# Kernel optimization log

Hardware: AMD Instinct MI355X
Metric: run time of the kernel (lower is better)

The kernel has to match this reference:

```python
import jax, jax.numpy as jnp
import numpy as np

EPS = 1e-12  # F.normalize default eps

def _unfold3(x):
    # torch F.unfold(kernel=(3,3), padding=1): [B,C,H,W] -> [B, C*9, H*W]
    # channel-major, kernel offsets row-major (matches torch ordering)
    B, C, H, W = x.shape
    xp = jnp.pad(x, ((0, 0), (0, 0), (1, 1), (1, 1)))
    p = jnp.stack([xp[:, :, i:i + H, j:j + W] for i in range(3) for j in range(3)], axis=2)  # [B,C,9,H,W]
    return p.reshape(B, C * 9, H * W)

def _fold3(u, H, W):
    # torch F.fold(output_size=(H,W), kernel=(3,3), padding=1): sums overlapping patches
    B, CK, L = u.shape
    C = CK // 9
    p = u.reshape(B, C, 3, 3, H, W)
    out = jnp.zeros((B, C, H + 2, W + 2), u.dtype)
    for i in range(3):
        for j in range(3):
            out = out.at[:, :, i:i + H, j:j + W].add(p[:, :, i, j])
    return out[:, :, 1:H + 1, 1:W + 1]

def setup_inputs() -> dict:
    key = jax.random.key(0)
    k1, k2, k3 = jax.random.split(key, 3)
    B, C, H, W = 4, 64, 64, 64
    return {
        "lrsr_lv3": jax.random.normal(k1, (B, C, H, W), jnp.float32),
        "refsr_lv3": jax.random.normal(k2, (B, C, H, W), jnp.float32),
        "ref_lv3": jax.random.normal(k3, (B, C, H, W), jnp.float32),
    }

def reference(lrsr_lv3, refsr_lv3, ref_lv3):
    B, C, H, W = lrsr_lv3.shape
    lr_u = _unfold3(lrsr_lv3)                         # [B, D, L_lr], D = C*9
    rs_u = _unfold3(refsr_lv3).transpose(0, 2, 1)     # [B, L_ref, D]
    rs_u = rs_u / jnp.maximum(jnp.linalg.norm(rs_u, axis=2, keepdims=True), EPS)
    lr_u = lr_u / jnp.maximum(jnp.linalg.norm(lr_u, axis=1, keepdims=True), EPS)
    corr = jnp.einsum('brd,bdl->brl', rs_u, lr_u)     # [B, L_ref, L_lr]
    s = jnp.max(corr, axis=1)                         # [B, L_lr]
    arg = jnp.argmax(corr, axis=1)                    # [B, L_lr]
    ref_u = _unfold3(ref_lv3)                         # [B, D, L_ref]
    trans_u = jnp.take_along_axis(ref_u, arg[:, None, :], axis=2)  # [B, D, L_lr]
    trans_lv3 = _fold3(trans_u, H, W)                 # [B, C, H, W]
    return s.reshape(B, 1, H, W), trans_lv3
```

## Files before the change

kernel.cpp:

```cpp
#include <hip/hip_runtime.h>

#define BATCH 4
#define CH    64
#define HH    64
#define WW    64
#define LL    4096
#define SPLITS 8
#define RPS   512
#define BM    128
#define BN    128
#define NRT   (RPS/BM)

#define RSTB  96
#define BUFB  24576
#define BSOFF 12288
#define CSTRIDE 139392

#define PAD_L   4356
#define GP_BYTE_BASE 1376256
#define GP_SIDE_STRIDE 6690816
#define GP_B_STRIDE    1672704
#define GP_COMP_STRIDE 557568
#define GP_TOTAL       13381632

#define WS_SSQ_RS 0
#define WS_SSQ_LR 16384
#define WS_INV_RS 32768
#define WS_INV_LR 49152
#define WS_PMAX   65536
#define WS_PARG   196608
#define WS_ARG    327680

typedef __attribute__((ext_vector_type(8))) short short8b;
typedef __attribute__((ext_vector_type(4))) float f32x4;
typedef __attribute__((ext_vector_type(16))) float f32x16;

__device__ __forceinline__ void gload16(const void* g, void* l) {
    __builtin_amdgcn_global_load_lds(
        (const __attribute__((address_space(1))) unsigned int*)g,
        (__attribute__((address_space(3))) unsigned int*)l, 16, 0, 0);
}

__global__ void k_split(const float* __restrict__ lrsr,
                        const float* __restrict__ refsr,
                        float* __restrict__ ws) {
    int tid  = threadIdx.x;
    int pos  = blockIdx.x * 256 + tid;
    int c8   = blockIdx.y;
    int side = blockIdx.z >> 2;
    int b    = blockIdx.z & 3;
    const float* src = (side ? lrsr : refsr) + (size_t)b * CH * LL + c8 * 8 * LL + pos;
    int ppos = (pos >> 6) * 66 + (pos & 63) + 67;
    char* dst = (char*)ws + GP_BYTE_BASE + side * GP_SIDE_STRIDE + b * GP_B_STRIDE
              + (size_t)(c8 * PAD_L + ppos) * 16;
    union { unsigned short u[8]; uint4 v; } w0, w1, w2;
    #pragma unroll
    for (int cc = 0; cc < 8; ++cc) {
        float x = src[cc * LL];
        unsigned u0 = __float_as_uint(x);
        float f0 = __uint_as_float(u0 & 0xffff0000u);
        float r1 = x - f0;
        unsigned u1 = __float_as_uint(r1);
        float f1 = __uint_as_float(u1 & 0xffff0000u);
        float r2 = r1 - f1;
        w0.u[cc] = (unsigned short)(u0 >> 16);
        w1.u[cc] = (unsigned short)(u1 >> 16);
        w2.u[cc] = (unsigned short)(__float_as_uint(r2) >> 16);
    }
    *(uint4*)(dst)                      = w0.v;
    *(uint4*)(dst + GP_COMP_STRIDE)     = w1.v;
    *(uint4*)(dst + 2 * GP_COMP_STRIDE) = w2.v;
}

__global__ void k_ssq(const float* __restrict__ lrsr,
                      const float* __restrict__ refsr,
                      float* __restrict__ ws) {
    int t = blockIdx.x * 256 + threadIdx.x;
    int b = t >> 12;
    int r = t & (LL - 1);
    const float* pl = lrsr + (size_t)b * CH * LL + r;
    const float* pr = refsr + (size_t)b * CH * LL + r;
    float sl = 0.f, sr = 0.f;
    #pragma unroll 8
    for (int c = 0; c < CH; ++c) {
        float a = pl[c * LL]; sl += a * a;
        float d = pr[c * LL]; sr += d * d;
    }
    ws[WS_SSQ_RS + t] = sr;
    ws[WS_SSQ_LR + t] = sl;
}

__global__ void k_inv(float* __restrict__ ws) {
    int t = blockIdx.x * 256 + threadIdx.x;
    int b = t >> 12;
    int r = t & (LL - 1);
    int y = r >> 6, x = r & 63;
    float srs = 0.f, slr = 0.f;
    for (int di = -1; di <= 1; ++di) {
        int yy = y + di;
        if ((unsigned)yy >= (unsigned)HH) continue;
        for (int dj = -1; dj <= 1; ++dj) {
            int xx = x + dj;
            if ((unsigned)xx >= (unsigned)WW) continue;
            int idx = b * LL + yy * WW + xx;
            srs += ws[WS_SSQ_RS + idx];
            slr += ws[WS_SSQ_LR + idx];
        }
    }
    ws[WS_INV_RS + t] = 1.f / fmaxf(sqrtf(srs), 1e-12f);
    ws[WS_INV_LR + t] = 1.f / fmaxf(sqrtf(slr), 1e-12f);
}

__global__ __launch_bounds__(256, 3)
void k_corrmax(float* __restrict__ ws) {
    __shared__ __align__(16) char LDSB[2 * BUFB];

    int tid  = threadIdx.x;
    int b    = blockIdx.z;
    int bx   = blockIdx.x;
    int l0   = bx * BN;
    int rbs  = blockIdx.y * RPS;

    int lane = tid & 63;
    int w    = tid >> 6;
    int wr   = w >> 1;
    int wc   = w & 1;
    int l31  = lane & 31;
    int g2   = lane >> 5;

    const float* invn_rs = ws + WS_INV_RS + b * LL;
    const char*  gpB = (const char*)ws + GP_BYTE_BASE + b * GP_B_STRIDE;
    int sB = w & 1;
    const char* bp = gpB + sB * GP_SIDE_STRIDE;

    int LCb[6];
    #pragma unroll
    for (int n = 0; n < 6; ++n) {
        int gg   = (n * 2 + (w >> 1)) * 64 + lane;
        int row  = gg / 6;
        int slot = gg - row * 6;
        int comp = slot >> 1;
        int oct  = slot & 1;
        LCb[n] = comp * GP_COMP_STRIDE + oct * (PAD_L * 16)
               + (row + 2 * (row >> 6)) * 16;
    }
    int ldsw = sB * BSOFF + (w >> 1) * 1024;

    int abase = (wr * 64 + l31) * RSTB + g2 * 16;
    int bbase = BSOFF + (wc * 64 + l31) * RSTB + g2 * 16;

    int yb = rbs >> 6;
    int yB = bx * 2;

    auto issue = [&](int rt2, int q2, int m2, int bufo) {
        int i2 = (q2 < 3) ? -1 : ((q2 < 6) ? 0 : 1);
        int j2 = q2 - (i2 + 1) * 3 - 1;
        int suA = ((yb + rt2 * 2 + 1 + i2) * 66 + 1 + j2) * 16 + m2 * CSTRIDE;
        int suB = ((yB + 1 + i2) * 66 + 1 + j2) * 16 + m2 * CSTRIDE;
        int su  = sB ? suB : suA;
        #pragma unroll
        for (int n = 0; n < 6; ++n)
            gload16(bp + (LCb[n] + su), LDSB + bufo + ldsw + n * 2048);
    };

    float rm[2] = {-1e30f, -1e30f};
    int   ra[2] = {0, 0};

    issue(0, 0, 0, 0);
    __syncthreads();

    int cur = 0;
    for (int rt = 0; rt < NRT; ++rt) {
        int r0 = rbs + rt * BM;

        f32x16 acc[2][2];
        #pragma unroll
        for (int mf = 0; mf < 2; ++mf)
            #pragma unroll
            for (int nf = 0; nf < 2; ++nf)
                #pragma unroll
                for (int e = 0; e < 16; ++e) acc[mf][nf][e] = 0.f;

        for (int q = 0; q < 9; ++q) {
            #pragma unroll
            for (int m = 0; m < 4; ++m) {
                if (!(rt == NRT - 1 && q == 8 && m == 3)) {
                    int m2 = m + 1, q2 = q, rt2 = rt;
                    if (m2 == 4) { m2 = 0; ++q2; if (q2 == 9) { q2 = 0; ++rt2; } }
                    issue(rt2, q2, m2, (cur ^ 1) * BUFB);
                }
                const char* lb = LDSB + cur * BUFB;
                short8b a[2][3], bv[2][3];
                #pragma unroll
                for (int mf = 0; mf < 2; ++mf)
                    #pragma unroll
                    for (int c = 0; c < 3; ++c)
                        a[mf][c] = *(const short8b*)(lb + abase + mf * 3072 + c * 32);
                #pragma unroll
                for (int nf = 0; nf < 2; ++nf)
                    #pragma unroll
                    for (int c = 0; c < 3; ++c)
                        bv[nf][c] = *(const short8b*)(lb + bbase + nf * 3072 + c * 32);
                __builtin_amdgcn_s_setprio(1);
                #pragma unroll
                for (int mf = 0; mf < 2; ++mf)
                    #pragma unroll
                    for (int nf = 0; nf < 2; ++nf) {
                        f32x16 d = acc[mf][nf];
                        d = __builtin_amdgcn_mfma_f32_32x32x16_bf16(a[mf][0], bv[nf][0], d, 0, 0, 0);
                        d = __builtin_amdgcn_mfma_f32_32x32x16_bf16(a[mf][0], bv[nf][1], d, 0, 0, 0);
                        d = __builtin_amdgcn_mfma_f32_32x32x16_bf16(a[mf][1], bv[nf][0], d, 0, 0, 0);
                        d = __builtin_amdgcn_mfma_f32_32x32x16_bf16(a[mf][1], bv[nf][1], d, 0, 0, 0);
                        d = __builtin_amdgcn_mfma_f32_32x32x16_bf16(a[mf][0], bv[nf][2], d, 0, 0, 0);
                        d = __builtin_amdgcn_mfma_f32_32x32x16_bf16(a[mf][2], bv[nf][0], d, 0, 0, 0);
                        acc[mf][nf] = d;
                    }
                __builtin_amdgcn_s_setprio(0);
                __syncthreads();
                cur ^= 1;
            }
        }

        f32x4 inv4[2][4];
        #pragma unroll
        for (int mf = 0; mf < 2; ++mf)
            #pragma unroll
            for (int rb = 0; rb < 4; ++rb)
                inv4[mf][rb] = *(const f32x4*)&invn_rs[r0 + wr * 64 + mf * 32 + g2 * 4 + rb * 8];
        #pragma unroll
        for (int nf = 0; nf < 2; ++nf)
            #pragma unroll
            for (int mf = 0; mf < 2; ++mf)
                #pragma unroll
                for (int reg = 0; reg < 16; ++reg) {
                    int r = r0 + wr * 64 + mf * 32 + (reg & 3) + 8 * (reg >> 2) + 4 * g2;
                    float val = acc[mf][nf][reg] * inv4[mf][reg >> 2][reg & 3];
                    if (val > rm[nf] || (val == rm[nf] && r < ra[nf])) { rm[nf] = val; ra[nf] = r; }
                }
    }

    #pragma unroll
    for (int nf = 0; nf < 2; ++nf) {
        float ov = __shfl_xor(rm[nf], 32);
        int   oi = __shfl_xor(ra[nf], 32);
        if (ov > rm[nf] || (ov == rm[nf] && oi < ra[nf])) { rm[nf] = ov; ra[nf] = oi; }
    }
    __syncthreads();
    float* sm2 = (float*)LDSB;
    int*   si2 = (int*)LDSB + 256;
    if (lane < 32) {
        #pragma unroll
        for (int nf = 0; nf < 2; ++nf) {
            sm2[wr * 128 + wc * 64 + nf * 32 + l31] = rm[nf];
            si2[wr * 128 + wc * 64 + nf * 32 + l31] = ra[nf];
        }
    }
    __syncthreads();
    if (tid < 128) {
        float bm = sm2[tid]; int ba = si2[tid];
        float v  = sm2[128 + tid]; int a2 = si2[128 + tid];
        if (v > bm || (v == bm && a2 < ba)) { bm = v; ba = a2; }
        int l = l0 + tid;
        int o = (b * SPLITS + blockIdx.y) * LL + l;
        ws[WS_PMAX + o] = bm;
        ((int*)ws)[WS_PARG + o] = ba;
    }
}

__global__ void k_reduce(float* __restrict__ ws, float* __restrict__ out) {
    int t = blockIdx.x * 256 + threadIdx.x;
    int b = t >> 12;
    int l = t & (LL - 1);
    float bm = -1e30f; int ba = 0;
    for (int s = 0; s < SPLITS; ++s) {
        int o = (b * SPLITS + s) * LL + l;
        float v = ws[WS_PMAX + o];
        int   a = ((int*)ws)[WS_PARG + o];
        if (v > bm || (v == bm && a < ba)) { bm = v; ba = a; }
    }
    out[t] = bm * ws[WS_INV_LR + t];
    ((int*)ws)[WS_ARG + t] = ba;
}

__global__ void k_fold(const float* __restrict__ ref,
                       const float* __restrict__ ws,
                       float* __restrict__ out) {
    int t = blockIdx.x * 256 + threadIdx.x;
    int b = t >> 18;
    int c = (t >> 12) & 63;
    int yx = t & (LL - 1);
    int y = yx >> 6, x = yx & 63;
    const int* ab = ((const int*)ws) + WS_ARG + b * LL;
    const float* rb = ref + (size_t)b * CH * LL + c * LL;
    float s = 0.f;
    #pragma unroll
    for (int i = 0; i < 3; ++i) {
        int yp = y + 1 - i;
        if ((unsigned)yp >= (unsigned)HH) continue;
        #pragma unroll
        for (int j = 0; j < 3; ++j) {
            int xp = x + 1 - j;
            if ((unsigned)xp >= (unsigned)WW) continue;
            int r = ab[yp * WW + xp];
            int ry = (r >> 6) + i - 1;
            int rx = (r & 63) + j - 1;
            if ((unsigned)ry < (unsigned)HH && (unsigned)rx < (unsigned)WW)
                s += rb[ry * WW + rx];
        }
    }
    out[BATCH * LL + t] = s;
}

extern "C" void kernel_launch(void* const* d_in, const int* in_sizes, int n_in,
                              void* d_out, int out_size, void* d_ws, size_t ws_size,
                              hipStream_t stream) {
    const float* lrsr = (const float*)d_in[0];
    const float* refsr = (const float*)d_in[1];
    const float* ref  = (const float*)d_in[2];
    float* out = (float*)d_out;
    float* ws  = (float*)d_ws;

    hipMemsetAsync((char*)d_ws + GP_BYTE_BASE, 0, GP_TOTAL, stream);
    k_split<<<dim3(16, 8, 8), dim3(256), 0, stream>>>(lrsr, refsr, ws);
    k_ssq<<<dim3(BATCH * LL / 256), dim3(256), 0, stream>>>(lrsr, refsr, ws);
    k_inv<<<dim3(BATCH * LL / 256), dim3(256), 0, stream>>>(ws);
    k_corrmax<<<dim3(LL / BN, SPLITS, BATCH), dim3(256), 0, stream>>>(ws);
    k_reduce<<<dim3(BATCH * LL / 256), dim3(256), 0, stream>>>(ws, out);
    k_fold<<<dim3(BATCH * CH * LL / 256), dim3(256), 0, stream>>>(ref, ws, out);
}
```

Measured before the change: 465.2 us.

## Enlarge corrmax tiles to 256x256 with 512-thread blocks and fewer splits

Reworks the correlation/argmax kernel to use 256x256 output tiles computed by 8 waves (each owning a 128x64 sub-tile, four M fragments), halving the row splits from 8 to 4. The LDS staging stride is padded to 112 bytes and the load mapping is rewritten so all 512 threads cooperatively fill both A and B tiles, with the barrier moved to the top of each step. The aim is higher arithmetic intensity per LDS byte and fewer global loads and partial results. In exchange it uses more LDS and registers per block, and launches only 256 blocks, which may underfill the GPU.

```diff
diff --git a/kernel.cpp b/kernel.cpp
--- a/kernel.cpp
+++ b/kernel.cpp
@@ -5,19 +5,17 @@
 #define HH    64
 #define WW    64
 #define LL    4096
-#define SPLITS 8
-#define RPS   512
-#define BM    128
-#define BN    128
-#define NRT   (RPS/BM)
-
-#define RSTB  96
-#define BUFB  24576
-#define BSOFF 12288
+#define SPLITS 4
+#define RPS   1024
+#define NRT   4
+
+#define RSTB  112
+#define BUFB  57344
+#define BSOFF 28672
 #define CSTRIDE 139392
 
 #define PAD_L   4356
-#define GP_BYTE_BASE 1376256
+#define GP_BYTE_BASE 1048576
 #define GP_SIDE_STRIDE 6690816
 #define GP_B_STRIDE    1672704
 #define GP_COMP_STRIDE 557568
@@ -28,8 +26,8 @@
 #define WS_INV_RS 32768
 #define WS_INV_LR 49152
 #define WS_PMAX   65536
-#define WS_PARG   196608
-#define WS_ARG    327680
+#define WS_PARG   131072
+#define WS_ARG    196608
 
 typedef __attribute__((ext_vector_type(8))) short short8b;
 typedef __attribute__((ext_vector_type(4))) float f32x4;
@@ -111,132 +109,136 @@
     ws[WS_INV_LR + t] = 1.f / fmaxf(sqrtf(slr), 1e-12f);
 }
 
-__global__ __launch_bounds__(256, 3)
+__global__ __launch_bounds__(512, 2)
 void k_corrmax(float* __restrict__ ws) {
     __shared__ __align__(16) char LDSB[2 * BUFB];
 
     int tid  = threadIdx.x;
     int b    = blockIdx.z;
     int bx   = blockIdx.x;
-    int l0   = bx * BN;
-    int rbs  = blockIdx.y * RPS;
+    int by   = blockIdx.y;
+    int l0   = bx * 256;
+    int rbs  = by * RPS;
 
     int lane = tid & 63;
-    int w    = tid >> 6;
-    int wr   = w >> 1;
-    int wc   = w & 1;
+    int w    = __builtin_amdgcn_readfirstlane(tid >> 6);
+    int wr   = w >> 2;
+    int wc   = w & 3;
     int l31  = lane & 31;
     int g2   = lane >> 5;
 
     const float* invn_rs = ws + WS_INV_RS + b * LL;
     const char*  gpB = (const char*)ws + GP_BYTE_BASE + b * GP_B_STRIDE;
-    int sB = w & 1;
-    const char* bp = gpB + sB * GP_SIDE_STRIDE;
-
-    int LCb[6];
+
+    int LC[7];
+    int sideF[7];
     #pragma unroll
-    for (int n = 0; n < 6; ++n) {
-        int gg   = (n * 2 + (w >> 1)) * 64 + lane;
-        int row  = gg / 6;
-        int slot = gg - row * 6;
-        int comp = slot >> 1;
-        int oct  = slot & 1;
-        LCb[n] = comp * GP_COMP_STRIDE + oct * (PAD_L * 16)
-               + (row + 2 * (row >> 6)) * 16;
-    }
-    int ldsw = sB * BSOFF + (w >> 1) * 1024;
-
-    int abase = (wr * 64 + l31) * RSTB + g2 * 16;
+    for (int n = 0; n < 7; ++n) {
+        int G    = n * 512 + tid;
+        int side = (n * 8 + w >= 28) ? 1 : 0;
+        int gg   = G - side * 1792;
+        int row  = gg / 7;
+        int slot = gg - row * 7;
+        int comp = (slot >= 6) ? 0 : (slot >> 1);
+        int oct  = (slot >= 6) ? 0 : (slot & 1);
+        LC[n] = side * GP_SIDE_STRIDE + comp * GP_COMP_STRIDE + oct * (PAD_L * 16)
+              + (row + 2 * (row >> 6)) * 16;
+        sideF[n] = side;
+    }
+
+    int abase = (wr * 128 + l31) * RSTB + g2 * 16;
     int bbase = BSOFF + (wc * 64 + l31) * RSTB + g2 * 16;
 
-    int yb = rbs >> 6;
-    int yB = bx * 2;
+    int ybA = by * 16;
+    int ybB = bx * 4;
 
     auto issue = [&](int rt2, int q2, int m2, int bufo) {
         int i2 = (q2 < 3) ? -1 : ((q2 < 6) ? 0 : 1);
         int j2 = q2 - (i2 + 1) * 3 - 1;
-        int suA = ((yb + rt2 * 2 + 1 + i2) * 66 + 1 + j2) * 16 + m2 * CSTRIDE;
-        int suB = ((yB + 1 + i2) * 66 + 1 + j2) * 16 + m2 * CSTRIDE;
-        int su  = sB ? suB : suA;
-        #pragma unroll
-        for (int n = 0; n < 6; ++n)
-            gload16(bp + (LCb[n] + su), LDSB + bufo + ldsw + n * 2048);
+        int suA = ((ybA + rt2 * 4 + 1 + i2) * 66 + 1 + j2) * 16 + m2 * CSTRIDE;
+        int suB = ((ybB + 1 + i2) * 66 + 1 + j2) * 16 + m2 * CSTRIDE;
+        #pragma unroll
+        for (int n = 0; n < 7; ++n) {
+            int su = sideF[n] ? suB : suA;
+            gload16(gpB + (LC[n] + su), LDSB + bufo + n * 8192 + tid * 16);
+        }
     };
 
     float rm[2] = {-1e30f, -1e30f};
     int   ra[2] = {0, 0};
 
     issue(0, 0, 0, 0);
-    __syncthreads();
-
     int cur = 0;
+
     for (int rt = 0; rt < NRT; ++rt) {
-        int r0 = rbs + rt * BM;
-
-        f32x16 acc[2][2];
-        #pragma unroll
-        for (int mf = 0; mf < 2; ++mf)
+        int r0 = rbs + rt * 256;
+
+        f32x16 acc[4][2];
+        #pragma unroll
+        for (int mf = 0; mf < 4; ++mf)
             #pragma unroll
             for (int nf = 0; nf < 2; ++nf)
                 #pragma unroll
                 for (int e = 0; e < 16; ++e) acc[mf][nf][e] = 0.f;
 
         for (int q = 0; q < 9; ++q) {
-            #pragma unroll
             for (int m = 0; m < 4; ++m) {
-                if (!(rt == NRT - 1 && q == 8 && m == 3)) {
+                __syncthreads();
+                {
                     int m2 = m + 1, q2 = q, rt2 = rt;
                     if (m2 == 4) { m2 = 0; ++q2; if (q2 == 9) { q2 = 0; ++rt2; } }
-                    issue(rt2, q2, m2, (cur ^ 1) * BUFB);
+                    if (rt2 < NRT) issue(rt2, q2, m2, (cur ^ 1) * BUFB);
                 }
                 const char* lb = LDSB + cur * BUFB;
-                short8b a[2][3], bv[2][3];
-                #pragma unroll
-                for (int mf = 0; mf < 2; ++mf)
-                    #pragma unroll
-                    for (int c = 0; c < 3; ++c)
-                        a[mf][c] = *(const short8b*)(lb + abase + mf * 3072 + c * 32);
+                short8b bfr[2][3];
                 #pragma unroll
                 for (int nf = 0; nf < 2; ++nf)
                     #pragma unroll
                     for (int c = 0; c < 3; ++c)
-                        bv[nf][c] = *(const short8b*)(lb + bbase + nf * 3072 + c * 32);
-                __builtin_amdgcn_s_setprio(1);
+                        bfr[nf][c] = *(const short8b*)(lb + bbase + nf * (32 * RSTB) + c * 32);
                 #pragma unroll
-                for (int mf = 0; mf < 2; ++mf)
+                for (int mfh = 0; mfh < 2; ++mfh) {
+                    short8b afr[2][3];
                     #pragma unroll
-                    for (int nf = 0; nf < 2; ++nf) {
-                        f32x16 d = acc[mf][nf];
-                        d = __builtin_amdgcn_mfma_f32_32x32x16_bf16(a[mf][0], bv[nf][0], d, 0, 0, 0);
-                        d = __builtin_amdgcn_mfma_f32_32x32x16_bf16(a[mf][0], bv[nf][1], d, 0, 0, 0);
-                        d = __builtin_amdgcn_mfma_f32_32x32x16_bf16(a[mf][1], bv[nf][0], d, 0, 0, 0);
-                        d = __builtin_amdgcn_mfma_f32_32x32x16_bf16(a[mf][1], bv[nf][1], d, 0, 0, 0);
-                        d = __builtin_amdgcn_mfma_f32_32x32x16_bf16(a[mf][0], bv[nf][2], d, 0, 0, 0);
-                        d = __builtin_amdgcn_mfma_f32_32x32x16_bf16(a[mf][2], bv[nf][0], d, 0, 0, 0);
-                        acc[mf][nf] = d;
-                    }
-                __builtin_amdgcn_s_setprio(0);
-                __syncthreads();
+                    for (int mi = 0; mi < 2; ++mi)
+                        #pragma unroll
+                        for (int c = 0; c < 3; ++c)
+                            afr[mi][c] = *(const short8b*)(lb + abase + (mfh * 2 + mi) * (32 * RSTB) + c * 32);
+                    __builtin_amdgcn_s_setprio(1);
+                    #pragma unroll
+                    for (int mi = 0; mi < 2; ++mi)
+                        #pragma unroll
+                        for (int nf = 0; nf < 2; ++nf) {
+                            f32x16 d = acc[mfh * 2 + mi][nf];
+                            d = __builtin_amdgcn_mfma_f32_32x32x16_bf16(afr[mi][0], bfr[nf][0], d, 0, 0, 0);
+                            d = __builtin_amdgcn_mfma_f32_32x32x16_bf16(afr[mi][0], bfr[nf][1], d, 0, 0, 0);
+                            d = __builtin_amdgcn_mfma_f32_32x32x16_bf16(afr[mi][1], bfr[nf][0], d, 0, 0, 0);
+                            d = __builtin_amdgcn_mfma_f32_32x32x16_bf16(afr[mi][1], bfr[nf][1], d, 0, 0, 0);
+                            d = __builtin_amdgcn_mfma_f32_32x32x16_bf16(afr[mi][0], bfr[nf][2], d, 0, 0, 0);
+                            d = __builtin_amdgcn_mfma_f32_32x32x16_bf16(afr[mi][2], bfr[nf][0], d, 0, 0, 0);
+                            acc[mfh * 2 + mi][nf] = d;
+                        }
+                    __builtin_amdgcn_s_setprio(0);
+                }
                 cur ^= 1;
             }
         }
 
-        f32x4 inv4[2][4];
-        #pragma unroll
-        for (int mf = 0; mf < 2; ++mf)
+        #pragma unroll
+        for (int mf = 0; mf < 4; ++mf) {
+            f32x4 iv[4];
             #pragma unroll
             for (int rb = 0; rb < 4; ++rb)
-                inv4[mf][rb] = *(const f32x4*)&invn_rs[r0 + wr * 64 + mf * 32 + g2 * 4 + rb * 8];
-        #pragma unroll
-        for (int nf = 0; nf < 2; ++nf)
+                iv[rb] = *(const f32x4*)&invn_rs[r0 + wr * 128 + mf * 32 + g2 * 4 + rb * 8];
             #pragma unroll
-            for (int mf = 0; mf < 2; ++mf)
+            for (int nf = 0; nf < 2; ++nf)
                 #pragma unroll
                 for (int reg = 0; reg < 16; ++reg) {
-                    int r = r0 + wr * 64 + mf * 32 + (reg & 3) + 8 * (reg >> 2) + 4 * g2;
-                    float val = acc[mf][nf][reg] * inv4[mf][reg >> 2][reg & 3];
+                    int r = r0 + wr * 128 + mf * 32 + (reg & 3) + 8 * (reg >> 2) + 4 * g2;
+                    float val = acc[mf][nf][reg] * iv[reg >> 2][reg & 3];
                     if (val > rm[nf] || (val == rm[nf] && r < ra[nf])) { rm[nf] = val; ra[nf] = r; }
                 }
+        }
     }
 
     #pragma unroll
@@ -247,21 +249,21 @@
     }
     __syncthreads();
     float* sm2 = (float*)LDSB;
-    int*   si2 = (int*)LDSB + 256;
+    int*   si2 = (int*)LDSB + 512;
     if (lane < 32) {
         #pragma unroll
         for (int nf = 0; nf < 2; ++nf) {
-            sm2[wr * 128 + wc * 64 + nf * 32 + l31] = rm[nf];
-            si2[wr * 128 + wc * 64 + nf * 32 + l31] = ra[nf];
+            sm2[wr * 256 + wc * 64 + nf * 32 + l31] = rm[nf];
+            si2[wr * 256 + wc * 64 + nf * 32 + l31] = ra[nf];
         }
     }
     __syncthreads();
-    if (tid < 128) {
+    if (tid < 256) {
         float bm = sm2[tid]; int ba = si2[tid];
-        float v  = sm2[128 + tid]; int a2 = si2[128 + tid];
+        float v  = sm2[256 + tid]; int a2 = si2[256 + tid];
         if (v > bm || (v == bm && a2 < ba)) { bm = v; ba = a2; }
         int l = l0 + tid;
-        int o = (b * SPLITS + blockIdx.y) * LL + l;
+        int o = (b * SPLITS + by) * LL + l;
         ws[WS_PMAX + o] = bm;
         ((int*)ws)[WS_PARG + o] = ba;
     }
@@ -324,7 +326,7 @@
     k_split<<<dim3(16, 8, 8), dim3(256), 0, stream>>>(lrsr, refsr, ws);
     k_ssq<<<dim3(BATCH * LL / 256), dim3(256), 0, stream>>>(lrsr, refsr, ws);
     k_inv<<<dim3(BATCH * LL / 256), dim3(256), 0, stream>>>(ws);
-    k_corrmax<<<dim3(LL / BN, SPLITS, BATCH), dim3(256), 0, stream>>>(ws);
+    k_corrmax<<<dim3(16, SPLITS, BATCH), dim3(512), 0, stream>>>(ws);
     k_reduce<<<dim3(BATCH * LL / 256), dim3(256), 0, stream>>>(ws, out);
     k_fold<<<dim3(BATCH * CH * LL / 256), dim3(256), 0, stream>>>(ref, ws, out);
 }
```

Measured after the change: 404.5 us. -13.0%, faster.
